# Kernel optimization log

Hardware: AMD Instinct MI355X
Metric: run time of the kernel (lower is better)

Reference implementation:

```python
import jax, jax.numpy as jnp
import numpy as np

B, T, N, C_IN = 64, 48, 1000, 2
H = 64            # hidden_dim
EMB = 16          # emb_dim
HORIZON = 12
C_OUT = 1


def setup_inputs() -> dict:
    key = jax.random.key(0)
    ks = jax.random.split(key, 16)
    nrm = lambda k, shp, s: (jax.random.normal(k, shp, dtype=jnp.float32) * s)
    return {
        'x':   nrm(ks[0], (B, T, N, C_IN), 1.0),
        'E1':  nrm(ks[1], (N, EMB), 0.1),
        'E2':  nrm(ks[2], (N, EMB), 0.1),
        # layer 0: gc_x Linear(C_IN -> 4H), gc_h Linear(H -> 4H); torch weight layout [out,in]
        'Wx0': nrm(ks[3], (4 * H, C_IN), 0.05), 'bx0': jnp.zeros((4 * H,), jnp.float32),
        'Wh0': nrm(ks[4], (4 * H, H), 0.05),    'bh0': jnp.zeros((4 * H,), jnp.float32),
        # layer 1: gc_x Linear(H -> 4H), gc_h Linear(H -> 4H)
        'Wx1': nrm(ks[5], (4 * H, H), 0.05),    'bx1': jnp.zeros((4 * H,), jnp.float32),
        'Wh1': nrm(ks[6], (4 * H, H), 0.05),    'bh1': jnp.zeros((4 * H,), jnp.float32),
        # proj: Linear(H -> C_OUT * HORIZON)
        'Wp':  nrm(ks[7], (C_OUT * HORIZON, H), 0.05), 'bp': jnp.zeros((C_OUT * HORIZON,), jnp.float32),
    }


def _cell(xt, h_prev, c_prev, A, Wx, bx, Wh, bh):
    # gates = lin(A @ xt) + lin(A @ h_prev)   -> [B,N,4H]
    gates = (jnp.einsum('ij,bjc->bic', A, xt) @ Wx.T + bx
             + jnp.einsum('ij,bjh->bih', A, h_prev) @ Wh.T + bh)
    i, f, o, g = jnp.split(gates, 4, axis=-1)
    i, f, o = jax.nn.sigmoid(i), jax.nn.sigmoid(f), jax.nn.sigmoid(o)
    g = jnp.tanh(g)
    c_t = f * c_prev + i * g
    h_t = o * jnp.tanh(c_t)
    return h_t, c_t


def reference(x, E1, E2, Wx0, bx0, Wh0, bh0, Wx1, bx1, Wh1, bh1, Wp, bp):
    A = jax.nn.softmax(jax.nn.relu(E1 @ E2.T), axis=-1)  # [N,N]
    b = x.shape[0]
    zeros = jnp.zeros((b, N, H), x.dtype)

    def step(carry, xt):
        h0, c0, h1, c1 = carry
        h0, c0 = _cell(xt, h0, c0, A, Wx0, bx0, Wh0, bh0)
        h1, c1 = _cell(h0, h1, c1, A, Wx1, bx1, Wh1, bh1)
        return (h0, c0, h1, c1), None

    xs = jnp.transpose(x, (1, 0, 2, 3))  # [T,B,N,C]
    (h0, c0, h1, c1), _ = jax.lax.scan(step, (zeros, zeros, zeros, zeros), xs)
    out = h1 @ Wp.T + bp                              # [B,N,HORIZON*C_OUT]
    out = out.reshape(b, N, HORIZON, -1)
    return jnp.transpose(out, (0, 2, 1, 3))           # [B,HORIZON,N,C_OUT]
```

## Files before the change

kernel.cpp:

```cpp
#include <hip/hip_runtime.h>
#include <math.h>

typedef float f4 __attribute__((ext_vector_type(4)));
typedef _Float16 h4 __attribute__((ext_vector_type(4)));
typedef _Float16 h8 __attribute__((ext_vector_type(8)));

#define WS_AX    0
#define WS_AHC   6144000
#define WS_C0    14532608
#define WS_C1    18628608
#define WS_HTH   22724608
#define WS_HTL   26918912
#define WS_A16H  31113216
#define WS_A16L  31637504
#define WS_W0T   32161792
#define WS_W1T   32178176

__global__ __launch_bounds__(256) void compute_A(const float* __restrict__ E1,
                                                 const float* __restrict__ E2,
                                                 float* __restrict__ At)
{
    __shared__ double z[1000];
    __shared__ double red[256];
    __shared__ double e1[16];
    const int i = blockIdx.x;
    const int tid = threadIdx.x;
    if (tid < 16) e1[tid] = (double)E1[i * 16 + tid];
    __syncthreads();
    double lmax = -1e300;
    for (int j = tid; j < 1000; j += 256) {
        double s = 0.0;
        #pragma unroll
        for (int c = 0; c < 16; ++c) s += e1[c] * (double)E2[j * 16 + c];
        if (s < 0.0) s = 0.0;
        z[j] = s;
        if (s > lmax) lmax = s;
    }
    red[tid] = lmax; __syncthreads();
    for (int off = 128; off > 0; off >>= 1) {
        if (tid < off) red[tid] = fmax(red[tid], red[tid + off]);
        __syncthreads();
    }
    const double zmax = red[0];
    __syncthreads();
    double lsum = 0.0;
    for (int j = tid; j < 1000; j += 256) {
        double e = exp(z[j] - zmax);
        z[j] = e;
        lsum += e;
    }
    red[tid] = lsum; __syncthreads();
    for (int off = 128; off > 0; off >>= 1) {
        if (tid < off) red[tid] += red[tid + off];
        __syncthreads();
    }
    const double inv = 1.0 / red[0];
    for (int j = tid; j < 1000; j += 256)
        At[(size_t)j * 1000 + i] = (float)(z[j] * inv);
}

__global__ __launch_bounds__(256) void transpose_x(const float* __restrict__ x,
                                                   float* __restrict__ Xr)
{
    int o = blockIdx.x * 256 + threadIdx.x;
    if (o >= 6144000) return;
    int j = o / 6144;
    int r = o - j * 6144;
    int t = r >> 7;
    int q = r & 127;
    int b = q >> 1;
    int c = q & 1;
    Xr[o] = x[(((size_t)(b * 48 + t)) * 1000 + j) * 2 + c];
}

__global__ __launch_bounds__(256) void zero_kernel(float* __restrict__ p, int n4)
{
    int i = blockIdx.x * 256 + threadIdx.x;
    if (i < n4) { f4 z = {0.f, 0.f, 0.f, 0.f}; ((f4*)p)[i] = z; }
}

__global__ __launch_bounds__(256) void prep_w(const float* __restrict__ Wh0,
                                              const float* __restrict__ Wx1,
                                              const float* __restrict__ Wh1,
                                              float* __restrict__ W0T,
                                              float* __restrict__ W1T)
{
    int idx = blockIdx.x * 256 + threadIdx.x;
    if (idx < 16384) {
        int k = idx >> 8, o = idx & 255;
        W0T[idx] = Wh0[o * 64 + k];
    }
    int j = idx - 16384;
    if (j >= 0 && j < 32768) {
        int k = j >> 8, o = j & 255;
        W1T[j] = (k < 64) ? Wx1[o * 64 + k] : Wh1[o * 64 + (k - 64)];
    }
}

__global__ __launch_bounds__(256) void prep_A(const float* __restrict__ At,
                                              _Float16* __restrict__ Ahh,
                                              _Float16* __restrict__ All)
{
    int idx = blockIdx.x * 256 + threadIdx.x;
    int m = idx >> 10, k = idx & 1023;
    float v = (m < 1000 && k < 1000) ? At[(size_t)k * 1000 + m] : 0.f;
    _Float16 hi = (_Float16)v;
    Ahh[idx] = hi;
    All[idx] = (_Float16)((v - (float)hi) * 2048.f);
}

__global__ __launch_bounds__(256) void gemm1000(const float* __restrict__ At,
                                                const float* __restrict__ B,
                                                float* __restrict__ C,
                                                int ncols)
{
    __shared__ float As[8][64];
    __shared__ float Bs[8][128];
    const int tid = threadIdx.x;
    const int tx = tid & 15;
    const int ty = tid >> 4;
    const int row0 = blockIdx.x * 64;
    const int col0 = blockIdx.y * 128;
    const int lm = tid & 63;
    const int lk = tid >> 6;
    const int bcol = tid & 127;
    const int bk = tid >> 7;
    const bool arow_ok = (row0 + lm) < 1000;

    float acc[4][8];
    #pragma unroll
    for (int r = 0; r < 4; ++r)
        #pragma unroll
        for (int c = 0; c < 8; ++c) acc[r][c] = 0.f;

    for (int k0 = 0; k0 < 1000; k0 += 8) {
        float a0 = arow_ok ? At[(size_t)(k0 + lk) * 1000 + row0 + lm] : 0.f;
        float a1 = arow_ok ? At[(size_t)(k0 + lk + 4) * 1000 + row0 + lm] : 0.f;
        float bv[4];
        #pragma unroll
        for (int kk = 0; kk < 4; ++kk)
            bv[kk] = B[(size_t)(k0 + bk * 4 + kk) * ncols + col0 + bcol];
        __syncthreads();
        As[lk][lm] = a0;
        As[lk + 4][lm] = a1;
        #pragma unroll
        for (int kk = 0; kk < 4; ++kk) Bs[bk * 4 + kk][bcol] = bv[kk];
        __syncthreads();
        #pragma unroll
        for (int k = 0; k < 8; ++k) {
            f4 av = *(const f4*)&As[k][ty * 4];
            f4 b0 = *(const f4*)&Bs[k][tx * 8];
            f4 b1 = *(const f4*)&Bs[k][tx * 8 + 4];
            #pragma unroll
            for (int r = 0; r < 4; ++r) {
                float a = av[r];
                acc[r][0] = fmaf(a, b0[0], acc[r][0]);
                acc[r][1] = fmaf(a, b0[1], acc[r][1]);
                acc[r][2] = fmaf(a, b0[2], acc[r][2]);
                acc[r][3] = fmaf(a, b0[3], acc[r][3]);
                acc[r][4] = fmaf(a, b1[0], acc[r][4]);
                acc[r][5] = fmaf(a, b1[1], acc[r][5]);
                acc[r][6] = fmaf(a, b1[2], acc[r][6]);
                acc[r][7] = fmaf(a, b1[3], acc[r][7]);
            }
        }
    }
    #pragma unroll
    for (int r = 0; r < 4; ++r) {
        int row = row0 + ty * 4 + r;
        if (row < 1000) {
            f4 o0 = {acc[r][0], acc[r][1], acc[r][2], acc[r][3]};
            f4 o1 = {acc[r][4], acc[r][5], acc[r][6], acc[r][7]};
            *(f4*)&C[(size_t)row * ncols + col0 + tx * 8]     = o0;
            *(f4*)&C[(size_t)row * ncols + col0 + tx * 8 + 4] = o1;
        }
    }
}

#define GL16(srcp, dstoff) \
    __builtin_amdgcn_global_load_lds((const __attribute__((address_space(1))) unsigned int*)(srcp), \
        (__attribute__((address_space(3))) unsigned int*)(lds + (dstoff)), 16, 0, 0)

__device__ __forceinline__ int swzb(int row, int lg) {
    return row * 64 + ((lg ^ ((row ^ (row >> 2)) & 3)) << 4);
}

__global__ __launch_bounds__(256, 2) void gemm_m(
    const _Float16* __restrict__ Ahg, const _Float16* __restrict__ Alg,
    const _Float16* __restrict__ Bhg, const _Float16* __restrict__ Blg,
    float* __restrict__ Cout)
{
    __shared__ __align__(1024) char lds[24576];
    const int tid = threadIdx.x;
    const int lane = tid & 63;
    const int w = tid >> 6;
    const int lg = lane >> 4, l15 = lane & 15;
    const int xcd = blockIdx.x & 7;
    const int j = blockIdx.x >> 3;
    const int m0 = (j >> 3) * 64;
    const int n0 = (xcd * 8 + (j & 7)) * 128;

    const int r16 = lane >> 2;
    const int sd = lane & 3;
    const char* src[6];
    #pragma unroll
    for (int q = 0; q < 6; ++q) {
        const int c = w * 6 + q;
        int row;
        const _Float16* g;
        if (c < 4)       { row = (c)      * 16 + r16; g = Ahg + (size_t)(m0 + row) * 1024; }
        else if (c < 8)  { row = (c - 4)  * 16 + r16; g = Alg + (size_t)(m0 + row) * 1024; }
        else if (c < 16) { row = (c - 8)  * 16 + r16; g = Bhg + (size_t)(n0 + row) * 1024; }
        else             { row = (c - 16) * 16 + r16; g = Blg + (size_t)(n0 + row) * 1024; }
        const int cg = sd ^ ((row ^ (row >> 2)) & 3);
        src[q] = (const char*)(g + cg * 8);
    }

    f4 acc0[4][2], acc1[4][2];
    #pragma unroll
    for (int a = 0; a < 4; ++a)
        #pragma unroll
        for (int b = 0; b < 2; ++b) {
            acc0[a][b] = (f4){0.f, 0.f, 0.f, 0.f};
            acc1[a][b] = (f4){0.f, 0.f, 0.f, 0.f};
        }

    for (int ks = 0; ks < 32; ++ks) {
        const int kadv = ks * 64;
        #pragma unroll
        for (int q = 0; q < 6; ++q)
            GL16(src[q] + kadv, (w * 6 + q) * 1024);
        __syncthreads();

        h8 fa[4], fl[4], bh[2], bl[2];
        #pragma unroll
        for (int mf = 0; mf < 4; ++mf) {
            const int ob = swzb(mf * 16 + l15, lg);
            fa[mf] = *(const h8*)(lds + ob);
            fl[mf] = *(const h8*)(lds + 4096 + ob);
        }
        #pragma unroll
        for (int nf = 0; nf < 2; ++nf) {
            const int ob = swzb(w * 32 + nf * 16 + l15, lg);
            bh[nf] = *(const h8*)(lds + 8192 + ob);
            bl[nf] = *(const h8*)(lds + 16384 + ob);
        }
        __syncthreads();

        #pragma unroll
        for (int nf = 0; nf < 2; ++nf)
            #pragma unroll
            for (int mf = 0; mf < 4; ++mf) {
                acc0[mf][nf] = __builtin_amdgcn_mfma_f32_16x16x32_f16(fa[mf], bh[nf], acc0[mf][nf], 0, 0, 0);
                acc1[mf][nf] = __builtin_amdgcn_mfma_f32_16x16x32_f16(fa[mf], bl[nf], acc1[mf][nf], 0, 0, 0);
                acc1[mf][nf] = __builtin_amdgcn_mfma_f32_16x16x32_f16(fl[mf], bh[nf], acc1[mf][nf], 0, 0, 0);
            }
    }

    #pragma unroll
    for (int mf = 0; mf < 4; ++mf)
        #pragma unroll
        for (int nf = 0; nf < 2; ++nf) {
            const int row = m0 + mf * 16 + lg * 4;
            const int col = n0 + w * 32 + nf * 16 + l15;
            #pragma unroll
            for (int e = 0; e < 4; ++e)
                Cout[(size_t)(row + e) * 8192 + col] =
                    acc0[mf][nf][e] + acc1[mf][nf][e] * (1.f / 2048.f);
        }
}

__global__ __launch_bounds__(256) void gates_f(
    const float* __restrict__ AHC, int two,
    const float* __restrict__ WT,
    const float* __restrict__ b1, const float* __restrict__ b2,
    const float* __restrict__ AX, const float* __restrict__ WxE, int t,
    float* __restrict__ Cst,
    _Float16* __restrict__ HTh, _Float16* __restrict__ HTl, int nbase)
{
    __shared__ __align__(16) char smem[43520];
    float (*As)[68] = (float(*)[68])smem;
    float *Bs       = (float*)(smem + 8704);
    float *wx       = (float*)(smem + 41472);
    _Float16 (*Sh)[80] = (_Float16(*)[80])smem;
    _Float16 (*Sl)[80] = (_Float16(*)[80])(smem + 10240);
    const int tid = threadIdx.x;
    const int tx = tid & 15;
    const int ty = tid >> 4;
    const int i0 = (blockIdx.x >> 6) * 64;
    const int b  = blockIdx.x & 63;
    const int mrow = tid >> 3;
    const int f4i  = tid & 7;

    if (WxE && tid < 128) ((f4*)wx)[tid] = ((const f4*)WxE)[tid];

    f4 acc[4][4];
    #pragma unroll
    for (int r = 0; r < 4; ++r)
        #pragma unroll
        for (int gq = 0; gq < 4; ++gq) acc[r][gq] = (f4){0.f, 0.f, 0.f, 0.f};

    const int nchunk = two ? 4 : 2;
    for (int ch = 0; ch < nchunk; ++ch) {
        const int coff = ((ch < 2) ? 0 : 4096) + b * 64;
        const int koff = (ch & 1) * 32;
        f4 av0 = *(const f4*)&AHC[(size_t)(i0 + mrow) * 8192 + coff + koff + f4i * 4];
        f4 av1 = *(const f4*)&AHC[(size_t)(i0 + mrow + 32) * 8192 + coff + koff + f4i * 4];
        const float* wsrc = WT + ch * 8192;
        f4 bv[8];
        #pragma unroll
        for (int r = 0; r < 8; ++r) bv[r] = *(const f4*)&wsrc[(tid + r * 256) * 4];
        __syncthreads();
        #pragma unroll
        for (int j = 0; j < 4; ++j) {
            As[f4i * 4 + j][mrow]      = av0[j];
            As[f4i * 4 + j][mrow + 32] = av1[j];
        }
        #pragma unroll
        for (int r = 0; r < 8; ++r) *(f4*)&Bs[(tid + r * 256) * 4] = bv[r];
        __syncthreads();
        #pragma unroll
        for (int k = 0; k < 32; ++k) {
            f4 av = *(const f4*)&As[k][ty * 4];
            f4 bq[4];
            #pragma unroll
            for (int gq = 0; gq < 4; ++gq) bq[gq] = *(const f4*)&Bs[k * 256 + gq * 64 + tx * 4];
            #pragma unroll
            for (int rr = 0; rr < 4; ++rr)
                #pragma unroll
                for (int gq = 0; gq < 4; ++gq)
                    acc[rr][gq] += av[rr] * bq[gq];
        }
    }

    f4 bb[4];
    #pragma unroll
    for (int gq = 0; gq < 4; ++gq) {
        f4 v1 = *(const f4*)&b1[gq * 64 + tx * 4];
        f4 v2 = *(const f4*)&b2[gq * 64 + tx * 4];
        bb[gq] = v1 + v2;
    }

    f4 hreg[4];
    #pragma unroll
    for (int rr = 0; rr < 4; ++rr) {
        const int i = i0 + ty * 4 + rr;
        const bool valid = (i < 1000);
        f4 gv[4];
        #pragma unroll
        for (int gq = 0; gq < 4; ++gq) gv[gq] = acc[rr][gq] + bb[gq];
        if (WxE && valid) {
            float x0 = AX[(size_t)i * 6144 + t * 128 + b * 2 + 0];
            float x1 = AX[(size_t)i * 6144 + t * 128 + b * 2 + 1];
            #pragma unroll
            for (int gq = 0; gq < 4; ++gq)
                #pragma unroll
                for (int hh = 0; hh < 4; ++hh) {
                    int gc = gq * 64 + tx * 4 + hh;
                    gv[gq][hh] = fmaf(x0, wx[gc * 2 + 0],
                                 fmaf(x1, wx[gc * 2 + 1], gv[gq][hh]));
                }
        }
        f4 hnew = {0.f, 0.f, 0.f, 0.f};
        if (valid) {
            const size_t base = ((size_t)b * 1000 + i) * 64 + tx * 4;
            f4 cold = *(const f4*)&Cst[base];
            f4 cnew;
            #pragma unroll
            for (int hh = 0; hh < 4; ++hh) {
                float ig = 1.f / (1.f + expf(-gv[0][hh]));
                float fg = 1.f / (1.f + expf(-gv[1][hh]));
                float og = 1.f / (1.f + expf(-gv[2][hh]));
                float gg = tanhf(gv[3][hh]);
                float c  = fg * cold[hh] + ig * gg;
                cnew[hh] = c;
                hnew[hh] = og * tanhf(c);
            }
            *(f4*)&Cst[base] = cnew;
        }
        hreg[rr] = hnew;
    }

    __syncthreads();
    #pragma unroll
    for (int hh = 0; hh < 4; ++hh) {
        h4 vh, vl;
        #pragma unroll
        for (int rr = 0; rr < 4; ++rr) {
            float v = hreg[rr][hh];
            _Float16 hi = (_Float16)v;
            vh[rr] = hi;
            vl[rr] = (_Float16)((v - (float)hi) * 2048.f);
        }
        *(h4*)&Sh[tx * 4 + hh][ty * 4] = vh;
        *(h4*)&Sl[tx * 4 + hh][ty * 4] = vl;
    }
    __syncthreads();
    #pragma unroll
    for (int pass = 0; pass < 2; ++pass) {
        const int c = pass * 256 + tid;
        const int row = c >> 3;
        const int off = (c & 7) * 8;
        const size_t go = (size_t)(nbase + b * 64 + row) * 1024 + i0 + off;
        *(h8*)&HTh[go] = *(const h8*)&Sh[row][off];
        *(h8*)&HTl[go] = *(const h8*)&Sl[row][off];
    }
}

__global__ __launch_bounds__(256) void proj_f16(const _Float16* __restrict__ HTh,
                                                const _Float16* __restrict__ HTl,
                                                const float* __restrict__ Wpj,
                                                const float* __restrict__ bp,
                                                float* __restrict__ out)
{
    int i = blockIdx.x * 256 + threadIdx.x;
    if (i >= 1000) return;
    int b = blockIdx.y;
    float hv[64];
    #pragma unroll
    for (int h = 0; h < 64; ++h) {
        size_t o = (size_t)(4096 + b * 64 + h) * 1024 + i;
        hv[h] = (float)HTh[o] + (float)HTl[o] * (1.f / 2048.f);
    }
    #pragma unroll
    for (int hor = 0; hor < 12; ++hor) {
        float s = bp[hor];
        #pragma unroll
        for (int h = 0; h < 64; ++h) s = fmaf(hv[h], Wpj[hor * 64 + h], s);
        out[(size_t)(b * 12 + hor) * 1000 + i] = s;
    }
}

extern "C" void kernel_launch(void* const* d_in, const int* in_sizes, int n_in,
                              void* d_out, int out_size, void* d_ws, size_t ws_size,
                              hipStream_t stream)
{
    const float* x   = (const float*)d_in[0];
    const float* E1  = (const float*)d_in[1];
    const float* E2  = (const float*)d_in[2];
    const float* Wx0 = (const float*)d_in[3];
    const float* bx0 = (const float*)d_in[4];
    const float* Wh0 = (const float*)d_in[5];
    const float* bh0 = (const float*)d_in[6];
    const float* Wx1 = (const float*)d_in[7];
    const float* bx1 = (const float*)d_in[8];
    const float* Wh1 = (const float*)d_in[9];
    const float* bh1 = (const float*)d_in[10];
    const float* Wp  = (const float*)d_in[11];
    const float* bp  = (const float*)d_in[12];
    float* out = (float*)d_out;
    float* ws  = (float*)d_ws;

    float*    AX  = ws + WS_AX;
    float*    AHC = ws + WS_AHC;
    float*    C0  = ws + WS_C0;
    float*    C1  = ws + WS_C1;
    _Float16* HTh = (_Float16*)(ws + WS_HTH);
    _Float16* HTl = (_Float16*)(ws + WS_HTL);
    _Float16* Ah  = (_Float16*)(ws + WS_A16H);
    _Float16* Al  = (_Float16*)(ws + WS_A16L);
    float*    W0T = ws + WS_W0T;
    float*    W1T = ws + WS_W1T;
    float*    At  = ws + WS_C0;
    float*    Xr  = ws + WS_AHC;

    compute_A<<<1000, 256, 0, stream>>>(E1, E2, At);
    transpose_x<<<24000, 256, 0, stream>>>(x, Xr);
    gemm1000<<<dim3(16, 48), 256, 0, stream>>>(At, Xr, AX, 6144);
    prep_w<<<192, 256, 0, stream>>>(Wh0, Wx1, Wh1, W0T, W1T);
    prep_A<<<4096, 256, 0, stream>>>(At, Ah, Al);
    zero_kernel<<<8000, 256, 0, stream>>>(ws + WS_C0, 2048000);
    zero_kernel<<<8192, 256, 0, stream>>>(AHC, 2097152);
    zero_kernel<<<8192, 256, 0, stream>>>(ws + WS_HTH, 2097152);

    for (int t = 0; t < 48; ++t) {
        gates_f<<<1024, 256, 0, stream>>>(AHC, 0, W0T, bh0, bx0,
                                          AX, Wx0, t, C0, HTh, HTl, 0);
        gemm_m<<<1024, 256, 0, stream>>>(Ah, Al, HTh, HTl, AHC);
        gates_f<<<1024, 256, 0, stream>>>(AHC, 1, W1T, bh1, bx1,
                                          nullptr, nullptr, 0, C1, HTh, HTl, 4096);
    }
    proj_f16<<<dim3(4, 64), 256, 0, stream>>>(HTh, HTl, Wp, bp, out);
    (void)in_sizes; (void)n_in; (void)out_size; (void)ws_size;
}
```

Baseline: 8.184 ms.

## Fuse layer-1 gates at step t with layer-0 gates at step t+1

Adds a gates_c kernel that runs layer-1 gates for step t and layer-0 gates for step t+1 in one 2048-block launch. This is possible because both read the same A@[h0|h1] product written by gemm_m and write disjoint halves of the h buffers. The recurrence therefore needs two launches per step instead of three, with the first layer-0 step peeled out before the loop. The final iteration wastes one half-grid computing a wrapped layer-0 step whose result is never used. The three separate zeroing launches are also merged into one contiguous zero pass.

```diff
diff --git a/kernel.cpp b/kernel.cpp
--- a/kernel.cpp
+++ b/kernel.cpp
@@ -268,6 +268,156 @@
                 Cout[(size_t)(row + e) * 8192 + col] =
                     acc0[mf][nf][e] + acc1[mf][nf][e] * (1.f / 2048.f);
         }
+}
+
+__global__ __launch_bounds__(256) void gates_c(
+    const float* __restrict__ AHC,
+    const float* __restrict__ W1T, const float* __restrict__ W0T,
+    const float* __restrict__ bh1, const float* __restrict__ bx1,
+    const float* __restrict__ bh0, const float* __restrict__ bx0,
+    const float* __restrict__ AX, const float* __restrict__ Wx0E, int tnext,
+    float* __restrict__ C1, float* __restrict__ C0,
+    _Float16* __restrict__ HTh, _Float16* __restrict__ HTl)
+{
+    __shared__ __align__(16) char smem[43520];
+    float (*As)[68] = (float(*)[68])smem;
+    float *Bs       = (float*)(smem + 8704);
+    float *wx       = (float*)(smem + 41472);
+    _Float16 (*Sh)[80] = (_Float16(*)[80])smem;
+    _Float16 (*Sl)[80] = (_Float16(*)[80])(smem + 10240);
+
+    const int half = blockIdx.x >> 10;
+    const int bidx = blockIdx.x & 1023;
+    const int two  = half ^ 1;
+    const float* WT  = half ? W0T : W1T;
+    const float* b1  = half ? bh0 : bh1;
+    const float* b2  = half ? bx0 : bx1;
+    const float* WxE = half ? Wx0E : nullptr;
+    float* Cst = half ? C0 : C1;
+    const int nbase = half ? 0 : 4096;
+    const int t = tnext;
+
+    const int tid = threadIdx.x;
+    const int tx = tid & 15;
+    const int ty = tid >> 4;
+    const int i0 = (bidx >> 6) * 64;
+    const int b  = bidx & 63;
+    const int mrow = tid >> 3;
+    const int f4i  = tid & 7;
+
+    if (WxE && tid < 128) ((f4*)wx)[tid] = ((const f4*)WxE)[tid];
+
+    f4 acc[4][4];
+    #pragma unroll
+    for (int r = 0; r < 4; ++r)
+        #pragma unroll
+        for (int gq = 0; gq < 4; ++gq) acc[r][gq] = (f4){0.f, 0.f, 0.f, 0.f};
+
+    const int nchunk = two ? 4 : 2;
+    for (int ch = 0; ch < nchunk; ++ch) {
+        const int coff = ((ch < 2) ? 0 : 4096) + b * 64;
+        const int koff = (ch & 1) * 32;
+        f4 av0 = *(const f4*)&AHC[(size_t)(i0 + mrow) * 8192 + coff + koff + f4i * 4];
+        f4 av1 = *(const f4*)&AHC[(size_t)(i0 + mrow + 32) * 8192 + coff + koff + f4i * 4];
+        const float* wsrc = WT + ch * 8192;
+        f4 bv[8];
+        #pragma unroll
+        for (int r = 0; r < 8; ++r) bv[r] = *(const f4*)&wsrc[(tid + r * 256) * 4];
+        __syncthreads();
+        #pragma unroll
+        for (int j = 0; j < 4; ++j) {
+            As[f4i * 4 + j][mrow]      = av0[j];
+            As[f4i * 4 + j][mrow + 32] = av1[j];
+        }
+        #pragma unroll
+        for (int r = 0; r < 8; ++r) *(f4*)&Bs[(tid + r * 256) * 4] = bv[r];
+        __syncthreads();
+        #pragma unroll
+        for (int k = 0; k < 32; ++k) {
+            f4 av = *(const f4*)&As[k][ty * 4];
+            f4 bq[4];
+            #pragma unroll
+            for (int gq = 0; gq < 4; ++gq) bq[gq] = *(const f4*)&Bs[k * 256 + gq * 64 + tx * 4];
+            #pragma unroll
+            for (int rr = 0; rr < 4; ++rr)
+                #pragma unroll
+                for (int gq = 0; gq < 4; ++gq)
+                    acc[rr][gq] += av[rr] * bq[gq];
+        }
+    }
+
+    f4 bb[4];
+    #pragma unroll
+    for (int gq = 0; gq < 4; ++gq) {
+        f4 v1 = *(const f4*)&b1[gq * 64 + tx * 4];
+        f4 v2 = *(const f4*)&b2[gq * 64 + tx * 4];
+        bb[gq] = v1 + v2;
+    }
+
+    f4 hreg[4];
+    #pragma unroll
+    for (int rr = 0; rr < 4; ++rr) {
+        const int i = i0 + ty * 4 + rr;
+        const bool valid = (i < 1000);
+        f4 gv[4];
+        #pragma unroll
+        for (int gq = 0; gq < 4; ++gq) gv[gq] = acc[rr][gq] + bb[gq];
+        if (WxE && valid) {
+            float x0 = AX[(size_t)i * 6144 + t * 128 + b * 2 + 0];
+            float x1 = AX[(size_t)i * 6144 + t * 128 + b * 2 + 1];
+            #pragma unroll
+            for (int gq = 0; gq < 4; ++gq)
+                #pragma unroll
+                for (int hh = 0; hh < 4; ++hh) {
+                    int gc = gq * 64 + tx * 4 + hh;
+                    gv[gq][hh] = fmaf(x0, wx[gc * 2 + 0],
+                                 fmaf(x1, wx[gc * 2 + 1], gv[gq][hh]));
+                }
+        }
+        f4 hnew = {0.f, 0.f, 0.f, 0.f};
+        if (valid) {
+            const size_t base = ((size_t)b * 1000 + i) * 64 + tx * 4;
+            f4 cold = *(const f4*)&Cst[base];
+            f4 cnew;
+            #pragma unroll
+            for (int hh = 0; hh < 4; ++hh) {
+                float ig = 1.f / (1.f + expf(-gv[0][hh]));
+                float fg = 1.f / (1.f + expf(-gv[1][hh]));
+                float og = 1.f / (1.f + expf(-gv[2][hh]));
+                float gg = tanhf(gv[3][hh]);
+                float c  = fg * cold[hh] + ig * gg;
+                cnew[hh] = c;
+                hnew[hh] = og * tanhf(c);
+            }
+            *(f4*)&Cst[base] = cnew;
+        }
+        hreg[rr] = hnew;
+    }
+
+    __syncthreads();
+    #pragma unroll
+    for (int hh = 0; hh < 4; ++hh) {
+        h4 vh, vl;
+        #pragma unroll
+        for (int rr = 0; rr < 4; ++rr) {
+            float v = hreg[rr][hh];
+            _Float16 hi = (_Float16)v;
+            vh[rr] = hi;
+            vl[rr] = (_Float16)((v - (float)hi) * 2048.f);
+        }
+        *(h4*)&Sh[tx * 4 + hh][ty * 4] = vh;
+        *(h4*)&Sl[tx * 4 + hh][ty * 4] = vl;
+    }
+    __syncthreads();
+    #pragma unroll
+    for (int pass = 0; pass < 2; ++pass) {
+        const int c = pass * 256 + tid;
+        const int row = c >> 3;
+        const int off = (c & 7) * 8;
+        const size_t go = (size_t)(nbase + b * 64 + row) * 1024 + i0 + off;
+        *(h8*)&HTh[go] = *(const h8*)&Sh[row][off];
+        *(h8*)&HTl[go] = *(const h8*)&Sl[row][off];
+    }
 }
 
 __global__ __launch_bounds__(256) void gates_f(
@@ -469,16 +619,14 @@
     gemm1000<<<dim3(16, 48), 256, 0, stream>>>(At, Xr, AX, 6144);
     prep_w<<<192, 256, 0, stream>>>(Wh0, Wx1, Wh1, W0T, W1T);
     prep_A<<<4096, 256, 0, stream>>>(At, Ah, Al);
-    zero_kernel<<<8000, 256, 0, stream>>>(ws + WS_C0, 2048000);
-    zero_kernel<<<8192, 256, 0, stream>>>(AHC, 2097152);
-    zero_kernel<<<8192, 256, 0, stream>>>(ws + WS_HTH, 2097152);
-
+    zero_kernel<<<24384, 256, 0, stream>>>(AHC, 6242304);
+
+    gates_f<<<1024, 256, 0, stream>>>(AHC, 0, W0T, bh0, bx0,
+                                      AX, Wx0, 0, C0, HTh, HTl, 0);
     for (int t = 0; t < 48; ++t) {
-        gates_f<<<1024, 256, 0, stream>>>(AHC, 0, W0T, bh0, bx0,
-                                          AX, Wx0, t, C0, HTh, HTl, 0);
         gemm_m<<<1024, 256, 0, stream>>>(Ah, Al, HTh, HTl, AHC);
-        gates_f<<<1024, 256, 0, stream>>>(AHC, 1, W1T, bh1, bx1,
-                                          nullptr, nullptr, 0, C1, HTh, HTl, 4096);
+        gates_c<<<2048, 256, 0, stream>>>(AHC, W1T, W0T, bh1, bx1, bh0, bx0,
+                                          AX, Wx0, (t + 1) & 47, C1, C0, HTh, HTl);
     }
     proj_f16<<<dim3(4, 64), 256, 0, stream>>>(HTh, HTl, Wp, bp, out);
     (void)in_sizes; (void)n_in; (void)out_size; (void)ws_size;
```

Result: no change. 8.039 ms (-1.8%).
